# Performance work log

Measured on AMD Instinct MI355X. Metric: run time of the kernel, lower is better.

The kernel has to match this reference:

```python
import jax, jax.numpy as jnp
import numpy as np
from math import sqrt

D_MODEL = 768
N_HEADS = 12
D_K = 64
D_V = 64
LN_EPS = 1e-5
NEG = -1e9


def layer_norm(x, g, b):
    mu = jnp.mean(x, axis=-1, keepdims=True)
    var = jnp.mean((x - mu) ** 2, axis=-1, keepdims=True)
    return (x - mu) * jax.lax.rsqrt(var + LN_EPS) * g + b


def setup_inputs() -> dict:
    key = jax.random.key(0)
    ks = jax.random.split(key, 8)
    B, S = 4, 1024
    pro1 = jax.random.normal(ks[0], (B, S, D_MODEL), dtype=jnp.float32)
    pro2 = jax.random.normal(ks[1], (B, S, D_MODEL), dtype=jnp.float32)
    # attn_mask is [B, H, S2, S1]; transpose(2,3) masks scores [B,H,S1,S2]
    mask1_2 = jax.random.bernoulli(ks[2], 0.3, (B, N_HEADS, S, S))
    sc = 1.0 / np.sqrt(D_MODEL)
    W_Q = jax.random.normal(ks[3], (D_MODEL, D_K * N_HEADS), dtype=jnp.float32) * sc
    W_K = jax.random.normal(ks[4], (D_MODEL, D_K * N_HEADS), dtype=jnp.float32) * sc
    fc1 = jax.random.normal(ks[5], (D_V * N_HEADS, D_MODEL), dtype=jnp.float32) * sc
    g1 = jnp.ones((D_MODEL,), jnp.float32)
    b1 = jnp.zeros((D_MODEL,), jnp.float32)
    g2 = jnp.ones((D_MODEL,), jnp.float32)
    b2 = jnp.zeros((D_MODEL,), jnp.float32)
    return {"pro1": pro1, "pro2": pro2, "mask1_2": mask1_2,
            "W_Q": W_Q, "W_K": W_K, "fc1": fc1,
            "g1": g1, "b1": b1, "g2": g2, "b2": b2}


def reference(pro1, pro2, mask1_2, W_Q, W_K, fc1, g1, b1, g2, b2):
    B, S1, _ = pro1.shape
    S2 = pro2.shape[1]
    # project and split heads: [B, H, S, d_k]
    Q = (pro1 @ W_Q).reshape(B, S1, N_HEADS, D_K).transpose(0, 2, 1, 3)
    K = (pro2 @ W_K).reshape(B, S2, N_HEADS, D_K).transpose(0, 2, 1, 3)
    scores = jnp.einsum('bhsd,bhtd->bhst', Q, K) / sqrt(D_K)  # [B,H,S1,S2]
    mask = jnp.swapaxes(mask1_2, 2, 3)  # attn_mask.transpose(2,3)
    scores = jnp.where(mask, NEG, scores)
    attn1 = jax.nn.softmax(scores, axis=-1)                  # over S2
    attn2 = jax.nn.softmax(jnp.swapaxes(scores, -1, -2), axis=-1)  # over S1
    ctx1 = jnp.einsum('bhst,bhtd->bhsd', attn1, K)  # [B,H,S1,d_k]
    ctx2 = jnp.einsum('bhts,bhsd->bhtd', attn2, Q)  # [B,H,S2,d_k]
    c1 = ctx1.transpose(0, 2, 1, 3).reshape(B, S1, N_HEADS * D_V)
    c2 = ctx2.transpose(0, 2, 1, 3).reshape(B, S2, N_HEADS * D_V)
    # NOTE: original applies fc1 to BOTH branches (fc2 is dead code)
    o1 = layer_norm(c1 @ fc1, g1, b1)
    o2 = layer_norm(c2 @ fc1, g2, b2)
    return (o1, o2)
```

## Files before the change

### kernel.cpp

```cpp
#include <hip/hip_runtime.h>
#include <hip/hip_bf16.h>
#include <stdint.h>

#define S 1024
#define DMODEL 768
#define NH 12
#define DK 64
#define BB 4
#define BH 48
#define M4 4096

typedef __attribute__((ext_vector_type(8))) short bf16x8;
typedef __attribute__((ext_vector_type(4))) float f32x4;
typedef __attribute__((ext_vector_type(4))) _Float16 f16x4;
typedef __attribute__((ext_vector_type(8))) _Float16 f16x8;

static __device__ __forceinline__ unsigned short f2bf(float f) {
  unsigned int u = __float_as_uint(f);
  unsigned int r = u + 0x7FFFu + ((u >> 16) & 1u);
  return (unsigned short)(r >> 16);
}
static __device__ __forceinline__ unsigned int pk2(float a, float b) {
  return (unsigned int)f2bf(a) | ((unsigned int)f2bf(b) << 16);
}
static __device__ __forceinline__ bf16x8 ldfrag(const unsigned short* p) {
  uint4 q = *reinterpret_cast<const uint4*>(p);
  return __builtin_bit_cast(bf16x8, q);
}
static __device__ __forceinline__ f16x8 ldfragh(const unsigned short* p) {
  uint4 q = *reinterpret_cast<const uint4*>(p);
  return __builtin_bit_cast(f16x8, q);
}
static __device__ __forceinline__ unsigned short h2u(_Float16 h) {
  return __builtin_bit_cast(unsigned short, h);
}

__global__ __launch_bounds__(256) void k_transpose(const float* w0, const float* w1, const float* w2,
                                                   unsigned short* o0, unsigned short* o1, unsigned short* o2) {
  const float* in = blockIdx.z == 0 ? w0 : (blockIdx.z == 1 ? w1 : w2);
  unsigned short* out = blockIdx.z == 0 ? o0 : (blockIdx.z == 1 ? o1 : o2);
  __shared__ float tile[32][33];
  int n0 = blockIdx.x * 32, k0 = blockIdx.y * 32;
  int tid = threadIdx.x;
  int r = tid >> 3, c = (tid & 7) * 4;
  float4 v = *reinterpret_cast<const float4*>(in + (size_t)(k0 + r) * DMODEL + n0 + c);
  tile[r][c] = v.x; tile[r][c + 1] = v.y; tile[r][c + 2] = v.z; tile[r][c + 3] = v.w;
  __syncthreads();
  ushort4 o;
  o.x = f2bf(tile[c + 0][r]);
  o.y = f2bf(tile[c + 1][r]);
  o.z = f2bf(tile[c + 2][r]);
  o.w = f2bf(tile[c + 3][r]);
  *reinterpret_cast<ushort4*>(out + (size_t)(n0 + r) * DMODEL + k0 + c) = o;
}

__global__ __launch_bounds__(256) void k_pack(const int* __restrict__ mask,
                                              unsigned int* __restrict__ mp2) {
  int bh = blockIdx.y;
  int w = threadIdx.x >> 6, lane = threadIdx.x & 63;
  int tile = blockIdx.x * 4 + w;
  int ti = tile >> 4, tj = tile & 15;
  int t0 = ti * 64, s0 = tj * 64;
  const int* mb = mask + (size_t)bh * S * S;
  unsigned long long rowword = 0;
#pragma unroll 8
  for (int r = 0; r < 64; ++r) {
    int v = mb[(size_t)(t0 + r) * S + s0 + lane];
    unsigned long long b = __ballot(v != 0);
    if (lane == r) rowword = b;
  }
  unsigned int* p2 = mp2 + (size_t)bh * 32 * S;
  p2[((s0 >> 5) + 0) * S + t0 + lane] = (unsigned int)rowword;
  p2[((s0 >> 5) + 1) * S + t0 + lane] = (unsigned int)(rowword >> 32);
}

__global__ __launch_bounds__(256, 2) void k_gemm128(
    int mode,
    const float* __restrict__ Af0, const float* __restrict__ Af1,
    const unsigned short* __restrict__ Ab0, const unsigned short* __restrict__ Ab1,
    const unsigned short* __restrict__ Bt0, const unsigned short* __restrict__ Bt1,
    unsigned short* __restrict__ oQ0, unsigned short* __restrict__ oQ1,
    unsigned short* __restrict__ oT0, unsigned short* __restrict__ oT1,
    float* __restrict__ oF0, float* __restrict__ oF1) {
  const float* Af = blockIdx.z ? Af1 : Af0;
  const unsigned short* Ab = blockIdx.z ? Ab1 : Ab0;
  const unsigned short* Bt = blockIdx.z ? Bt1 : Bt0;
  __shared__ __align__(16) unsigned short As[128 * 72];
  __shared__ __align__(16) unsigned short Bs[128 * 72];
  int tid = threadIdx.x;
  int m0 = blockIdx.x * 128, n0 = blockIdx.y * 128;
  int w = tid >> 6, lane = tid & 63, lane15 = lane & 15, quad = lane >> 4;
  int row0 = (w >> 1) * 64, col0 = (w & 1) * 64;
  f32x4 acc[4][4] = {};
  int sr = tid >> 2, sc = (tid & 3) * 16;
  const unsigned short* gB0 = Bt + (size_t)(n0 + sr) * DMODEL + sc;
  const unsigned short* gB1 = Bt + (size_t)(n0 + 64 + sr) * DMODEL + sc;
  uint4 vb[2][2];
  vb[0][0] = *reinterpret_cast<const uint4*>(gB0);
  vb[0][1] = *reinterpret_cast<const uint4*>(gB0 + 8);
  vb[1][0] = *reinterpret_cast<const uint4*>(gB1);
  vb[1][1] = *reinterpret_cast<const uint4*>(gB1 + 8);
  const float* gAf0 = Af + (size_t)(m0 + sr) * DMODEL + sc;
  const float* gAf1 = Af + (size_t)(m0 + 64 + sr) * DMODEL + sc;
  const unsigned short* gAb0 = Ab + (size_t)(m0 + sr) * DMODEL + sc;
  const unsigned short* gAb1 = Ab + (size_t)(m0 + 64 + sr) * DMODEL + sc;
  float4 fa[2][4];
  uint4 va[2][2];
  if (mode == 0) {
#pragma unroll
    for (int g = 0; g < 4; ++g) fa[0][g] = *reinterpret_cast<const float4*>(gAf0 + g * 4);
#pragma unroll
    for (int g = 0; g < 4; ++g) fa[1][g] = *reinterpret_cast<const float4*>(gAf1 + g * 4);
  } else {
    va[0][0] = *reinterpret_cast<const uint4*>(gAb0);
    va[0][1] = *reinterpret_cast<const uint4*>(gAb0 + 8);
    va[1][0] = *reinterpret_cast<const uint4*>(gAb1);
    va[1][1] = *reinterpret_cast<const uint4*>(gAb1 + 8);
  }
  for (int kc = 0; kc < 12; ++kc) {
    __syncthreads();
    if (mode == 0) {
#pragma unroll
      for (int h2 = 0; h2 < 2; ++h2) {
        uint4 u0, u1;
        u0.x = pk2(fa[h2][0].x, fa[h2][0].y); u0.y = pk2(fa[h2][0].z, fa[h2][0].w);
        u0.z = pk2(fa[h2][1].x, fa[h2][1].y); u0.w = pk2(fa[h2][1].z, fa[h2][1].w);
        u1.x = pk2(fa[h2][2].x, fa[h2][2].y); u1.y = pk2(fa[h2][2].z, fa[h2][2].w);
        u1.z = pk2(fa[h2][3].x, fa[h2][3].y); u1.w = pk2(fa[h2][3].z, fa[h2][3].w);
        *reinterpret_cast<uint4*>(&As[(h2 * 64 + sr) * 72 + sc]) = u0;
        *reinterpret_cast<uint4*>(&As[(h2 * 64 + sr) * 72 + sc + 8]) = u1;
      }
    } else {
#pragma unroll
      for (int h2 = 0; h2 < 2; ++h2) {
        *reinterpret_cast<uint4*>(&As[(h2 * 64 + sr) * 72 + sc]) = va[h2][0];
        *reinterpret_cast<uint4*>(&As[(h2 * 64 + sr) * 72 + sc + 8]) = va[h2][1];
      }
    }
#pragma unroll
    for (int h2 = 0; h2 < 2; ++h2) {
      *reinterpret_cast<uint4*>(&Bs[(h2 * 64 + sr) * 72 + sc]) = vb[h2][0];
      *reinterpret_cast<uint4*>(&Bs[(h2 * 64 + sr) * 72 + sc + 8]) = vb[h2][1];
    }
    if (kc < 11) {
      int k0 = (kc + 1) * 64;
      if (mode == 0) {
#pragma unroll
        for (int g = 0; g < 4; ++g) fa[0][g] = *reinterpret_cast<const float4*>(gAf0 + k0 + g * 4);
#pragma unroll
        for (int g = 0; g < 4; ++g) fa[1][g] = *reinterpret_cast<const float4*>(gAf1 + k0 + g * 4);
      } else {
        va[0][0] = *reinterpret_cast<const uint4*>(gAb0 + k0);
        va[0][1] = *reinterpret_cast<const uint4*>(gAb0 + k0 + 8);
        va[1][0] = *reinterpret_cast<const uint4*>(gAb1 + k0);
        va[1][1] = *reinterpret_cast<const uint4*>(gAb1 + k0 + 8);
      }
      vb[0][0] = *reinterpret_cast<const uint4*>(gB0 + k0);
      vb[0][1] = *reinterpret_cast<const uint4*>(gB0 + k0 + 8);
      vb[1][0] = *reinterpret_cast<const uint4*>(gB1 + k0);
      vb[1][1] = *reinterpret_cast<const uint4*>(gB1 + k0 + 8);
    }
    __syncthreads();
#pragma unroll
    for (int ks = 0; ks < 2; ++ks) {
      int kk = ks * 32 + quad * 8;
      bf16x8 a[4], b[4];
#pragma unroll
      for (int i = 0; i < 4; ++i) a[i] = ldfrag(&As[(row0 + i * 16 + lane15) * 72 + kk]);
#pragma unroll
      for (int j = 0; j < 4; ++j) b[j] = ldfrag(&Bs[(col0 + j * 16 + lane15) * 72 + kk]);
#pragma unroll
      for (int i = 0; i < 4; ++i)
#pragma unroll
        for (int j = 0; j < 4; ++j)
          acc[i][j] = __builtin_amdgcn_mfma_f32_16x16x32_bf16(a[i], b[j], acc[i][j], 0, 0, 0);
    }
  }
  if (mode == 0) {
    unsigned short* out = blockIdx.z ? oQ1 : oQ0;
    unsigned short* outT = blockIdx.z ? oT1 : oT0;
    f16x4 iden;
#pragma unroll
    for (int i = 0; i < 4; ++i) iden[i] = (_Float16)((quad * 4 + i) == lane15 ? 1.0f : 0.0f);
    f32x4 zero4 = {};
#pragma unroll
    for (int i = 0; i < 4; ++i)
#pragma unroll
      for (int j = 0; j < 4; ++j) {
        f16x4 cf;
#pragma unroll
        for (int reg = 0; reg < 4; ++reg) cf[reg] = (_Float16)acc[i][j][reg];
        f32x4 tq = __builtin_amdgcn_mfma_f32_16x16x16f16(cf, iden, zero4, 0, 0, 0);
        {
          int m = m0 + row0 + i * 16 + lane15;
          int n = n0 + col0 + j * 16 + quad * 4;
          int b = m >> 10, s = m & 1023, h = n >> 6, d = n & 63;
          ushort4 o;
          o.x = h2u((_Float16)tq[0]); o.y = h2u((_Float16)tq[1]);
          o.z = h2u((_Float16)tq[2]); o.w = h2u((_Float16)tq[3]);
          *reinterpret_cast<ushort4*>(&out[(((size_t)(b * NH + h)) * S + s) * DK + d]) = o;
        }
        {
          int n = n0 + col0 + j * 16 + lane15;
          int m = m0 + row0 + i * 16 + quad * 4;
          int b = m >> 10, s = m & 1023, h = n >> 6, d = n & 63;
          ushort4 o;
          o.x = h2u((_Float16)acc[i][j][0]); o.y = h2u((_Float16)acc[i][j][1]);
          o.z = h2u((_Float16)acc[i][j][2]); o.w = h2u((_Float16)acc[i][j][3]);
          *reinterpret_cast<ushort4*>(&outT[(((size_t)(b * NH + h)) * DK + d) * S + s]) = o;
        }
      }
  } else {
    float* out = blockIdx.z ? oF1 : oF0;
#pragma unroll
    for (int i = 0; i < 4; ++i)
#pragma unroll
      for (int j = 0; j < 4; ++j)
#pragma unroll
        for (int reg = 0; reg < 4; ++reg) {
          int m = m0 + row0 + i * 16 + quad * 4 + reg;
          int n = n0 + col0 + j * 16 + lane15;
          out[(size_t)m * DMODEL + n] = acc[i][j][reg];
        }
  }
}

__global__ __launch_bounds__(256, 3) void k_attn(
    const unsigned short* __restrict__ Qb, const unsigned short* __restrict__ Kb,
    const unsigned short* __restrict__ QT, const unsigned short* __restrict__ KT,
    const unsigned int* __restrict__ mp2,
    unsigned short* __restrict__ c1, unsigned short* __restrict__ c2) {
  int bh = blockIdx.y, path = blockIdx.z;
  int s0b = blockIdx.x * 128;
  const unsigned short* X = path ? Kb : Qb;
  const unsigned short* Y = path ? Qb : Kb;
  const unsigned short* YT = path ? QT : KT;
  unsigned short* outc = path ? c2 : c1;

  __shared__ __align__(16) unsigned short YS[64 * 72];
  __shared__ __align__(16) unsigned short YTS[64 * 72];
  __shared__ unsigned int MWS[256];

  const unsigned short* Xb = X + (size_t)bh * S * DK;
  const unsigned short* Yb = Y + (size_t)bh * S * DK;
  const unsigned short* YTb = YT + (size_t)bh * DK * S;
  const unsigned int* mbg = mp2 + (size_t)bh * 32 * S;

  int tid = threadIdx.x;
  int w = tid >> 6, lane = tid & 63, lane15 = lane & 15, quad = lane >> 4;
  int s0w = s0b + w * 32;

  f16x8 xf[2][2];
#pragma unroll
  for (int rg = 0; rg < 2; ++rg) {
    xf[rg][0] = ldfragh(Xb + (size_t)(s0w + rg * 16 + lane15) * DK + quad * 8);
    xf[rg][1] = ldfragh(Xb + (size_t)(s0w + rg * 16 + lane15) * DK + 32 + quad * 8);
  }

  int sr4 = tid >> 2, sc4 = (tid & 3) * 16;
  const unsigned short* gY = Yb + (size_t)sr4 * DK + sc4;
  const unsigned short* gYT = YTb + (size_t)sr4 * S + sc4;
  uint4 y0 = *reinterpret_cast<const uint4*>(gY);
  uint4 y1 = *reinterpret_cast<const uint4*>(gY + 8);
  uint4 t0 = *reinterpret_cast<const uint4*>(gYT);
  uint4 t1 = *reinterpret_cast<const uint4*>(gYT + 8);
  int mws_idx = (path == 0) ? ((tid & 63) * 4 + (tid >> 6)) : ((tid & 127) * 2 + (tid >> 7));
  unsigned int mwv = (path == 0)
      ? mbg[((size_t)((s0b >> 5) + (tid >> 6))) * S + (tid & 63)]
      : mbg[((size_t)(tid >> 7)) * S + s0b + (tid & 127)];

  f32x4 outa[2][4] = {};
  float lsum[2] = {0.f, 0.f};

  for (int jc = 0; jc < 16; ++jc) {
    __syncthreads();
    *reinterpret_cast<uint4*>(&YS[sr4 * 72 + sc4]) = y0;
    *reinterpret_cast<uint4*>(&YS[sr4 * 72 + sc4 + 8]) = y1;
    *reinterpret_cast<uint4*>(&YTS[sr4 * 72 + sc4]) = t0;
    *reinterpret_cast<uint4*>(&YTS[sr4 * 72 + sc4 + 8]) = t1;
    MWS[mws_idx] = mwv;
    {
      int jn = (jc + 1 < 16) ? (jc + 1) * 64 : jc * 64;
      y0 = *reinterpret_cast<const uint4*>(gY + (size_t)jn * DK);
      y1 = *reinterpret_cast<const uint4*>(gY + (size_t)jn * DK + 8);
      t0 = *reinterpret_cast<const uint4*>(gYT + jn);
      t1 = *reinterpret_cast<const uint4*>(gYT + jn + 8);
      mwv = (path == 0)
          ? mbg[((size_t)((s0b >> 5) + (tid >> 6))) * S + jn + (tid & 63)]
          : mbg[((size_t)((jn >> 5) + (tid >> 7))) * S + s0b + (tid & 127)];
    }
    __syncthreads();

    f32x4 scv[4][2];
#pragma unroll
    for (int st = 0; st < 4; ++st) {
      f16x8 a0 = ldfragh(&YS[(st * 16 + lane15) * 72 + quad * 8]);
      f16x8 a1 = ldfragh(&YS[(st * 16 + lane15) * 72 + 32 + quad * 8]);
#pragma unroll
      for (int rg = 0; rg < 2; ++rg) {
        f32x4 v = {};
        v = __builtin_amdgcn_mfma_f32_16x16x32_f16(a0, xf[rg][0], v, 0, 0, 0);
        v = __builtin_amdgcn_mfma_f32_16x16x32_f16(a1, xf[rg][1], v, 0, 0, 0);
        scv[st][rg] = v;
      }
    }
    f16x4 pfa[4][2];
    if (path == 0) {
#pragma unroll
      for (int st = 0; st < 4; ++st)
#pragma unroll
        for (int reg = 0; reg < 4; ++reg) {
          unsigned int wdv = MWS[(st * 16 + quad * 4 + reg) * 4 + w];
#pragma unroll
          for (int rg = 0; rg < 2; ++rg) {
            float e = __expf(scv[st][rg][reg] * 0.125f);
            float p = ((wdv >> (unsigned)(rg * 16 + lane15)) & 1u) ? 0.f : e;
            lsum[rg] += p;
            pfa[st][rg][reg] = (_Float16)p;
          }
        }
    } else {
#pragma unroll
      for (int rg = 0; rg < 2; ++rg) {
        unsigned int wv0 = MWS[(w * 32 + rg * 16 + lane15) * 2 + 0];
        unsigned int wv1 = MWS[(w * 32 + rg * 16 + lane15) * 2 + 1];
#pragma unroll
        for (int st = 0; st < 4; ++st) {
          unsigned int wdv = (st < 2) ? wv0 : wv1;
#pragma unroll
          for (int reg = 0; reg < 4; ++reg) {
            unsigned int sh = (unsigned)((st & 1) * 16 + quad * 4 + reg);
            float e = __expf(scv[st][rg][reg] * 0.125f);
            float p = ((wdv >> sh) & 1u) ? 0.f : e;
            lsum[rg] += p;
            pfa[st][rg][reg] = (_Float16)p;
          }
        }
      }
    }
#pragma unroll
    for (int st = 0; st < 4; ++st)
#pragma unroll
      for (int dsub = 0; dsub < 4; ++dsub) {
        uint2 q = *reinterpret_cast<const uint2*>(&YTS[(dsub * 16 + lane15) * 72 + st * 16 + quad * 4]);
        f16x4 yb = __builtin_bit_cast(f16x4, q);
#pragma unroll
        for (int rg = 0; rg < 2; ++rg)
          outa[rg][dsub] = __builtin_amdgcn_mfma_f32_16x16x16f16(pfa[st][rg], yb, outa[rg][dsub], 0, 0, 0);
      }
  }

#pragma unroll
  for (int rg = 0; rg < 2; ++rg) {
    lsum[rg] += __shfl_xor(lsum[rg], 16);
    lsum[rg] += __shfl_xor(lsum[rg], 32);
  }
  float rinv[2][4];
#pragma unroll
  for (int rg = 0; rg < 2; ++rg)
#pragma unroll
    for (int reg = 0; reg < 4; ++reg)
      rinv[rg][reg] = 1.0f / __shfl(lsum[rg], quad * 4 + reg);

  int b = bh / NH, h = bh % NH;
#pragma unroll
  for (int rg = 0; rg < 2; ++rg)
#pragma unroll
    for (int dsub = 0; dsub < 4; ++dsub)
#pragma unroll
      for (int reg = 0; reg < 4; ++reg) {
        float v = outa[rg][dsub][reg] * rinv[rg][reg];
        int srow = s0w + rg * 16 + quad * 4 + reg;
        size_t idx = ((size_t)(b * S) + srow) * DMODEL + h * DK + dsub * 16 + lane15;
        outc[idx] = f2bf(v);
      }
}

__global__ __launch_bounds__(256) void k_ln(const float* __restrict__ f1, const float* __restrict__ f2,
                                            const float* __restrict__ g1, const float* __restrict__ b1,
                                            const float* __restrict__ g2, const float* __restrict__ b2,
                                            float* __restrict__ out) {
  int rowg = blockIdx.x;
  int sel = rowg >> 12;
  int row = rowg & 4095;
  const float* in = sel ? f2 : f1;
  const float* g = sel ? g2 : g1;
  const float* be = sel ? b2 : b1;
  int tid = threadIdx.x;
  const float* p = in + (size_t)row * DMODEL;
  float x0 = p[tid], x1 = p[tid + 256], x2 = p[tid + 512];
  float s = x0 + x1 + x2;
  float ss = x0 * x0 + x1 * x1 + x2 * x2;
#pragma unroll
  for (int m = 1; m < 64; m <<= 1) { s += __shfl_xor(s, m); ss += __shfl_xor(ss, m); }
  __shared__ float ps[4], pss[4];
  int w = tid >> 6;
  if ((tid & 63) == 0) { ps[w] = s; pss[w] = ss; }
  __syncthreads();
  s = ps[0] + ps[1] + ps[2] + ps[3];
  ss = pss[0] + pss[1] + pss[2] + pss[3];
  float mu = s * (1.0f / 768.0f);
  float var = ss * (1.0f / 768.0f) - mu * mu;
  float rstd = rsqrtf(var + 1e-5f);
  float* o = out + ((size_t)sel * M4 + row) * DMODEL;
  o[tid] = (x0 - mu) * rstd * g[tid] + be[tid];
  o[tid + 256] = (x1 - mu) * rstd * g[tid + 256] + be[tid + 256];
  o[tid + 512] = (x2 - mu) * rstd * g[tid + 512] + be[tid + 512];
}

extern "C" void kernel_launch(void* const* d_in, const int* in_sizes, int n_in,
                              void* d_out, int out_size, void* d_ws, size_t ws_size,
                              hipStream_t stream) {
  const float* pro1 = (const float*)d_in[0];
  const float* pro2 = (const float*)d_in[1];
  const int* mask = (const int*)d_in[2];
  const float* WQ = (const float*)d_in[3];
  const float* WK = (const float*)d_in[4];
  const float* FC1 = (const float*)d_in[5];
  const float* g1 = (const float*)d_in[6];
  const float* b1 = (const float*)d_in[7];
  const float* g2 = (const float*)d_in[8];
  const float* b2 = (const float*)d_in[9];
  float* out = (float*)d_out;
  char* ws = (char*)d_ws;

  float* f1 = (float*)(ws + 0);
  unsigned short* wqt = (unsigned short*)(ws + 12582912);
  unsigned short* wkt = (unsigned short*)(ws + 13762560);
  unsigned short* fc1t = (unsigned short*)(ws + 14942208);
  unsigned short* Qb = (unsigned short*)(ws + 16121856);
  unsigned short* Kb = (unsigned short*)(ws + 22413312);
  unsigned short* QT = (unsigned short*)(ws + 28704768);
  unsigned short* KT = (unsigned short*)(ws + 34996224);
  unsigned int* mp2 = (unsigned int*)(ws + 41287680);
  float* f2 = (float*)(ws + 47579136);
  unsigned short* c1 = (unsigned short*)(ws + 60162048);
  unsigned short* c2 = (unsigned short*)(ws + 66453504);

  k_transpose<<<dim3(24, 24, 3), 256, 0, stream>>>(WQ, WK, FC1, wqt, wkt, fc1t);
  k_pack<<<dim3(64, BH), 256, 0, stream>>>(mask, mp2);
  k_gemm128<<<dim3(32, 6, 2), 256, 0, stream>>>(0, pro1, pro2, nullptr, nullptr, wqt, wkt,
                                                Qb, Kb, QT, KT, nullptr, nullptr);
  k_attn<<<dim3(8, BH, 2), 256, 0, stream>>>(Qb, Kb, QT, KT, mp2, c1, c2);
  k_gemm128<<<dim3(32, 6, 2), 256, 0, stream>>>(1, nullptr, nullptr, c1, c2, fc1t, fc1t,
                                                nullptr, nullptr, nullptr, nullptr, f1, f2);
  k_ln<<<8192, 256, 0, stream>>>(f1, f2, g1, b1, g2, b2, out);
}
```

Baseline: 474.4 us.

## Shrink GEMM and attention tiles, pre-convert inputs to bf16

The fp32 activations are now converted to bf16 in a separate pass, so the projection GEMM loads bf16 directly. The GEMM M tile is halved to 64 rows and the attention query tile to 64 rows (16 per wave), with launch bounds raised to 4 blocks per CU. This doubles the number of blocks and cuts per-thread register use, aiming for more occupancy and better CU fill on the large chip. The cost is two extra conversion launches, an extra read/write of the inputs, and more re-reading of the B/K tiles across the larger grid.

```diff
diff --git a/kernel.cpp b/kernel.cpp
--- a/kernel.cpp
+++ b/kernel.cpp
@@ -20,9 +20,6 @@
   unsigned int r = u + 0x7FFFu + ((u >> 16) & 1u);
   return (unsigned short)(r >> 16);
 }
-static __device__ __forceinline__ unsigned int pk2(float a, float b) {
-  return (unsigned int)f2bf(a) | ((unsigned int)f2bf(b) << 16);
-}
 static __device__ __forceinline__ bf16x8 ldfrag(const unsigned short* p) {
   uint4 q = *reinterpret_cast<const uint4*>(p);
   return __builtin_bit_cast(bf16x8, q);
@@ -33,6 +30,17 @@
 }
 static __device__ __forceinline__ unsigned short h2u(_Float16 h) {
   return __builtin_bit_cast(unsigned short, h);
+}
+
+__global__ __launch_bounds__(256) void k_convert(const float* __restrict__ in,
+                                                 unsigned short* __restrict__ out, int n4) {
+  int i = blockIdx.x * 256 + threadIdx.x;
+  if (i < n4) {
+    float4 v = reinterpret_cast<const float4*>(in)[i];
+    ushort4 o;
+    o.x = f2bf(v.x); o.y = f2bf(v.y); o.z = f2bf(v.z); o.w = f2bf(v.w);
+    reinterpret_cast<ushort4*>(out)[i] = o;
+  }
 }
 
 __global__ __launch_bounds__(256) void k_transpose(const float* w0, const float* w1, const float* w2,
@@ -74,87 +82,45 @@
   p2[((s0 >> 5) + 1) * S + t0 + lane] = (unsigned int)(rowword >> 32);
 }
 
-__global__ __launch_bounds__(256, 2) void k_gemm128(
+__global__ __launch_bounds__(256, 4) void k_gemm(
     int mode,
-    const float* __restrict__ Af0, const float* __restrict__ Af1,
-    const unsigned short* __restrict__ Ab0, const unsigned short* __restrict__ Ab1,
+    const unsigned short* __restrict__ A0, const unsigned short* __restrict__ A1,
     const unsigned short* __restrict__ Bt0, const unsigned short* __restrict__ Bt1,
     unsigned short* __restrict__ oQ0, unsigned short* __restrict__ oQ1,
     unsigned short* __restrict__ oT0, unsigned short* __restrict__ oT1,
     float* __restrict__ oF0, float* __restrict__ oF1) {
-  const float* Af = blockIdx.z ? Af1 : Af0;
-  const unsigned short* Ab = blockIdx.z ? Ab1 : Ab0;
+  const unsigned short* A = blockIdx.z ? A1 : A0;
   const unsigned short* Bt = blockIdx.z ? Bt1 : Bt0;
-  __shared__ __align__(16) unsigned short As[128 * 72];
+  __shared__ __align__(16) unsigned short As[64 * 72];
   __shared__ __align__(16) unsigned short Bs[128 * 72];
   int tid = threadIdx.x;
-  int m0 = blockIdx.x * 128, n0 = blockIdx.y * 128;
+  int m0 = blockIdx.x * 64, n0 = blockIdx.y * 128;
   int w = tid >> 6, lane = tid & 63, lane15 = lane & 15, quad = lane >> 4;
-  int row0 = (w >> 1) * 64, col0 = (w & 1) * 64;
-  f32x4 acc[4][4] = {};
+  int row0 = (w >> 1) * 32, col0 = (w & 1) * 64;
+  f32x4 acc[2][4] = {};
   int sr = tid >> 2, sc = (tid & 3) * 16;
+  const unsigned short* gA = A + (size_t)(m0 + sr) * DMODEL + sc;
   const unsigned short* gB0 = Bt + (size_t)(n0 + sr) * DMODEL + sc;
   const unsigned short* gB1 = Bt + (size_t)(n0 + 64 + sr) * DMODEL + sc;
+  uint4 va0 = *reinterpret_cast<const uint4*>(gA);
+  uint4 va1 = *reinterpret_cast<const uint4*>(gA + 8);
   uint4 vb[2][2];
   vb[0][0] = *reinterpret_cast<const uint4*>(gB0);
   vb[0][1] = *reinterpret_cast<const uint4*>(gB0 + 8);
   vb[1][0] = *reinterpret_cast<const uint4*>(gB1);
   vb[1][1] = *reinterpret_cast<const uint4*>(gB1 + 8);
-  const float* gAf0 = Af + (size_t)(m0 + sr) * DMODEL + sc;
-  const float* gAf1 = Af + (size_t)(m0 + 64 + sr) * DMODEL + sc;
-  const unsigned short* gAb0 = Ab + (size_t)(m0 + sr) * DMODEL + sc;
-  const unsigned short* gAb1 = Ab + (size_t)(m0 + 64 + sr) * DMODEL + sc;
-  float4 fa[2][4];
-  uint4 va[2][2];
-  if (mode == 0) {
-#pragma unroll
-    for (int g = 0; g < 4; ++g) fa[0][g] = *reinterpret_cast<const float4*>(gAf0 + g * 4);
-#pragma unroll
-    for (int g = 0; g < 4; ++g) fa[1][g] = *reinterpret_cast<const float4*>(gAf1 + g * 4);
-  } else {
-    va[0][0] = *reinterpret_cast<const uint4*>(gAb0);
-    va[0][1] = *reinterpret_cast<const uint4*>(gAb0 + 8);
-    va[1][0] = *reinterpret_cast<const uint4*>(gAb1);
-    va[1][1] = *reinterpret_cast<const uint4*>(gAb1 + 8);
-  }
   for (int kc = 0; kc < 12; ++kc) {
     __syncthreads();
-    if (mode == 0) {
-#pragma unroll
-      for (int h2 = 0; h2 < 2; ++h2) {
-        uint4 u0, u1;
-        u0.x = pk2(fa[h2][0].x, fa[h2][0].y); u0.y = pk2(fa[h2][0].z, fa[h2][0].w);
-        u0.z = pk2(fa[h2][1].x, fa[h2][1].y); u0.w = pk2(fa[h2][1].z, fa[h2][1].w);
-        u1.x = pk2(fa[h2][2].x, fa[h2][2].y); u1.y = pk2(fa[h2][2].z, fa[h2][2].w);
-        u1.z = pk2(fa[h2][3].x, fa[h2][3].y); u1.w = pk2(fa[h2][3].z, fa[h2][3].w);
-        *reinterpret_cast<uint4*>(&As[(h2 * 64 + sr) * 72 + sc]) = u0;
-        *reinterpret_cast<uint4*>(&As[(h2 * 64 + sr) * 72 + sc + 8]) = u1;
-      }
-    } else {
-#pragma unroll
-      for (int h2 = 0; h2 < 2; ++h2) {
-        *reinterpret_cast<uint4*>(&As[(h2 * 64 + sr) * 72 + sc]) = va[h2][0];
-        *reinterpret_cast<uint4*>(&As[(h2 * 64 + sr) * 72 + sc + 8]) = va[h2][1];
-      }
-    }
-#pragma unroll
-    for (int h2 = 0; h2 < 2; ++h2) {
-      *reinterpret_cast<uint4*>(&Bs[(h2 * 64 + sr) * 72 + sc]) = vb[h2][0];
-      *reinterpret_cast<uint4*>(&Bs[(h2 * 64 + sr) * 72 + sc + 8]) = vb[h2][1];
-    }
+    *reinterpret_cast<uint4*>(&As[sr * 72 + sc]) = va0;
+    *reinterpret_cast<uint4*>(&As[sr * 72 + sc + 8]) = va1;
+    *reinterpret_cast<uint4*>(&Bs[sr * 72 + sc]) = vb[0][0];
+    *reinterpret_cast<uint4*>(&Bs[sr * 72 + sc + 8]) = vb[0][1];
+    *reinterpret_cast<uint4*>(&Bs[(64 + sr) * 72 + sc]) = vb[1][0];
+    *reinterpret_cast<uint4*>(&Bs[(64 + sr) * 72 + sc + 8]) = vb[1][1];
     if (kc < 11) {
       int k0 = (kc + 1) * 64;
-      if (mode == 0) {
-#pragma unroll
-        for (int g = 0; g < 4; ++g) fa[0][g] = *reinterpret_cast<const float4*>(gAf0 + k0 + g * 4);
-#pragma unroll
-        for (int g = 0; g < 4; ++g) fa[1][g] = *reinterpret_cast<const float4*>(gAf1 + k0 + g * 4);
-      } else {
-        va[0][0] = *reinterpret_cast<const uint4*>(gAb0 + k0);
-        va[0][1] = *reinterpret_cast<const uint4*>(gAb0 + k0 + 8);
-        va[1][0] = *reinterpret_cast<const uint4*>(gAb1 + k0);
-        va[1][1] = *reinterpret_cast<const uint4*>(gAb1 + k0 + 8);
-      }
+      va0 = *reinterpret_cast<const uint4*>(gA + k0);
+      va1 = *reinterpret_cast<const uint4*>(gA + k0 + 8);
       vb[0][0] = *reinterpret_cast<const uint4*>(gB0 + k0);
       vb[0][1] = *reinterpret_cast<const uint4*>(gB0 + k0 + 8);
       vb[1][0] = *reinterpret_cast<const uint4*>(gB1 + k0);
@@ -164,13 +130,13 @@
 #pragma unroll
     for (int ks = 0; ks < 2; ++ks) {
       int kk = ks * 32 + quad * 8;
-      bf16x8 a[4], b[4];
-#pragma unroll
-      for (int i = 0; i < 4; ++i) a[i] = ldfrag(&As[(row0 + i * 16 + lane15) * 72 + kk]);
+      bf16x8 a[2], b[4];
+#pragma unroll
+      for (int i = 0; i < 2; ++i) a[i] = ldfrag(&As[(row0 + i * 16 + lane15) * 72 + kk]);
 #pragma unroll
       for (int j = 0; j < 4; ++j) b[j] = ldfrag(&Bs[(col0 + j * 16 + lane15) * 72 + kk]);
 #pragma unroll
-      for (int i = 0; i < 4; ++i)
+      for (int i = 0; i < 2; ++i)
 #pragma unroll
         for (int j = 0; j < 4; ++j)
           acc[i][j] = __builtin_amdgcn_mfma_f32_16x16x32_bf16(a[i], b[j], acc[i][j], 0, 0, 0);
@@ -184,7 +150,7 @@
     for (int i = 0; i < 4; ++i) iden[i] = (_Float16)((quad * 4 + i) == lane15 ? 1.0f : 0.0f);
     f32x4 zero4 = {};
 #pragma unroll
-    for (int i = 0; i < 4; ++i)
+    for (int i = 0; i < 2; ++i)
 #pragma unroll
       for (int j = 0; j < 4; ++j) {
         f16x4 cf;
@@ -213,7 +179,7 @@
   } else {
     float* out = blockIdx.z ? oF1 : oF0;
 #pragma unroll
-    for (int i = 0; i < 4; ++i)
+    for (int i = 0; i < 2; ++i)
 #pragma unroll
       for (int j = 0; j < 4; ++j)
 #pragma unroll
@@ -225,13 +191,13 @@
   }
 }
 
-__global__ __launch_bounds__(256, 3) void k_attn(
+__global__ __launch_bounds__(256, 4) void k_attn(
     const unsigned short* __restrict__ Qb, const unsigned short* __restrict__ Kb,
     const unsigned short* __restrict__ QT, const unsigned short* __restrict__ KT,
     const unsigned int* __restrict__ mp2,
     unsigned short* __restrict__ c1, unsigned short* __restrict__ c2) {
   int bh = blockIdx.y, path = blockIdx.z;
-  int s0b = blockIdx.x * 128;
+  int s0b = blockIdx.x * 64;
   const unsigned short* X = path ? Kb : Qb;
   const unsigned short* Y = path ? Qb : Kb;
   const unsigned short* YT = path ? QT : KT;
@@ -239,7 +205,7 @@
 
   __shared__ __align__(16) unsigned short YS[64 * 72];
   __shared__ __align__(16) unsigned short YTS[64 * 72];
-  __shared__ unsigned int MWS[256];
+  __shared__ unsigned int MWS[128];
 
   const unsigned short* Xb = X + (size_t)bh * S * DK;
   const unsigned short* Yb = Y + (size_t)bh * S * DK;
@@ -248,14 +214,10 @@
 
   int tid = threadIdx.x;
   int w = tid >> 6, lane = tid & 63, lane15 = lane & 15, quad = lane >> 4;
-  int s0w = s0b + w * 32;
-
-  f16x8 xf[2][2];
-#pragma unroll
-  for (int rg = 0; rg < 2; ++rg) {
-    xf[rg][0] = ldfragh(Xb + (size_t)(s0w + rg * 16 + lane15) * DK + quad * 8);
-    xf[rg][1] = ldfragh(Xb + (size_t)(s0w + rg * 16 + lane15) * DK + 32 + quad * 8);
-  }
+  int s0w = s0b + w * 16;
+
+  f16x8 xf0 = ldfragh(Xb + (size_t)(s0w + lane15) * DK + quad * 8);
+  f16x8 xf1 = ldfragh(Xb + (size_t)(s0w + lane15) * DK + 32 + quad * 8);
 
   int sr4 = tid >> 2, sc4 = (tid & 3) * 16;
   const unsigned short* gY = Yb + (size_t)sr4 * DK + sc4;
@@ -264,13 +226,14 @@
   uint4 y1 = *reinterpret_cast<const uint4*>(gY + 8);
   uint4 t0 = *reinterpret_cast<const uint4*>(gYT);
   uint4 t1 = *reinterpret_cast<const uint4*>(gYT + 8);
-  int mws_idx = (path == 0) ? ((tid & 63) * 4 + (tid >> 6)) : ((tid & 127) * 2 + (tid >> 7));
-  unsigned int mwv = (path == 0)
-      ? mbg[((size_t)((s0b >> 5) + (tid >> 6))) * S + (tid & 63)]
-      : mbg[((size_t)(tid >> 7)) * S + s0b + (tid & 127)];
-
-  f32x4 outa[2][4] = {};
-  float lsum[2] = {0.f, 0.f};
+  unsigned int mwv = 0;
+  if (tid < 128)
+    mwv = (path == 0)
+        ? mbg[((size_t)((s0b >> 5) + (tid & 1))) * S + (tid >> 1)]
+        : mbg[((size_t)(tid & 1)) * S + s0b + (tid >> 1)];
+
+  f32x4 outa[4] = {};
+  float lsum = 0.f;
 
   for (int jc = 0; jc < 16; ++jc) {
     __syncthreads();
@@ -278,63 +241,56 @@
     *reinterpret_cast<uint4*>(&YS[sr4 * 72 + sc4 + 8]) = y1;
     *reinterpret_cast<uint4*>(&YTS[sr4 * 72 + sc4]) = t0;
     *reinterpret_cast<uint4*>(&YTS[sr4 * 72 + sc4 + 8]) = t1;
-    MWS[mws_idx] = mwv;
+    if (tid < 128) MWS[tid] = mwv;
     {
       int jn = (jc + 1 < 16) ? (jc + 1) * 64 : jc * 64;
       y0 = *reinterpret_cast<const uint4*>(gY + (size_t)jn * DK);
       y1 = *reinterpret_cast<const uint4*>(gY + (size_t)jn * DK + 8);
       t0 = *reinterpret_cast<const uint4*>(gYT + jn);
       t1 = *reinterpret_cast<const uint4*>(gYT + jn + 8);
-      mwv = (path == 0)
-          ? mbg[((size_t)((s0b >> 5) + (tid >> 6))) * S + jn + (tid & 63)]
-          : mbg[((size_t)((jn >> 5) + (tid >> 7))) * S + s0b + (tid & 127)];
+      if (tid < 128)
+        mwv = (path == 0)
+            ? mbg[((size_t)((s0b >> 5) + (tid & 1))) * S + jn + (tid >> 1)]
+            : mbg[((size_t)((jn >> 5) + (tid & 1))) * S + s0b + (tid >> 1)];
     }
     __syncthreads();
 
-    f32x4 scv[4][2];
+    f32x4 scv[4];
 #pragma unroll
     for (int st = 0; st < 4; ++st) {
       f16x8 a0 = ldfragh(&YS[(st * 16 + lane15) * 72 + quad * 8]);
       f16x8 a1 = ldfragh(&YS[(st * 16 + lane15) * 72 + 32 + quad * 8]);
-#pragma unroll
-      for (int rg = 0; rg < 2; ++rg) {
-        f32x4 v = {};
-        v = __builtin_amdgcn_mfma_f32_16x16x32_f16(a0, xf[rg][0], v, 0, 0, 0);
-        v = __builtin_amdgcn_mfma_f32_16x16x32_f16(a1, xf[rg][1], v, 0, 0, 0);
-        scv[st][rg] = v;
-      }
-    }
-    f16x4 pfa[4][2];
+      f32x4 v = {};
+      v = __builtin_amdgcn_mfma_f32_16x16x32_f16(a0, xf0, v, 0, 0, 0);
+      v = __builtin_amdgcn_mfma_f32_16x16x32_f16(a1, xf1, v, 0, 0, 0);
+      scv[st] = v;
+    }
+    f16x4 pfa[4];
     if (path == 0) {
+      unsigned int sh = (unsigned)((w & 1) * 16 + lane15);
 #pragma unroll
       for (int st = 0; st < 4; ++st)
 #pragma unroll
         for (int reg = 0; reg < 4; ++reg) {
-          unsigned int wdv = MWS[(st * 16 + quad * 4 + reg) * 4 + w];
-#pragma unroll
-          for (int rg = 0; rg < 2; ++rg) {
-            float e = __expf(scv[st][rg][reg] * 0.125f);
-            float p = ((wdv >> (unsigned)(rg * 16 + lane15)) & 1u) ? 0.f : e;
-            lsum[rg] += p;
-            pfa[st][rg][reg] = (_Float16)p;
-          }
+          unsigned int wdv = MWS[(st * 16 + quad * 4 + reg) * 2 + (w >> 1)];
+          float e = __expf(scv[st][reg] * 0.125f);
+          float p = ((wdv >> sh) & 1u) ? 0.f : e;
+          lsum += p;
+          pfa[st][reg] = (_Float16)p;
         }
     } else {
-#pragma unroll
-      for (int rg = 0; rg < 2; ++rg) {
-        unsigned int wv0 = MWS[(w * 32 + rg * 16 + lane15) * 2 + 0];
-        unsigned int wv1 = MWS[(w * 32 + rg * 16 + lane15) * 2 + 1];
-#pragma unroll
-        for (int st = 0; st < 4; ++st) {
-          unsigned int wdv = (st < 2) ? wv0 : wv1;
-#pragma unroll
-          for (int reg = 0; reg < 4; ++reg) {
-            unsigned int sh = (unsigned)((st & 1) * 16 + quad * 4 + reg);
-            float e = __expf(scv[st][rg][reg] * 0.125f);
-            float p = ((wdv >> sh) & 1u) ? 0.f : e;
-            lsum[rg] += p;
-            pfa[st][rg][reg] = (_Float16)p;
-          }
+      unsigned int wv0 = MWS[(w * 16 + lane15) * 2 + 0];
+      unsigned int wv1 = MWS[(w * 16 + lane15) * 2 + 1];
+#pragma unroll
+      for (int st = 0; st < 4; ++st) {
+        unsigned int wdv = (st < 2) ? wv0 : wv1;
+#pragma unroll
+        for (int reg = 0; reg < 4; ++reg) {
+          unsigned int sh = (unsigned)((st & 1) * 16 + quad * 4 + reg);
+          float e = __expf(scv[st][reg] * 0.125f);
+          float p = ((wdv >> sh) & 1u) ? 0.f : e;
+          lsum += p;
+          pfa[st][reg] = (_Float16)p;
         }
       }
     }
@@ -344,36 +300,27 @@
       for (int dsub = 0; dsub < 4; ++dsub) {
         uint2 q = *reinterpret_cast<const uint2*>(&YTS[(dsub * 16 + lane15) * 72 + st * 16 + quad * 4]);
         f16x4 yb = __builtin_bit_cast(f16x4, q);
-#pragma unroll
-        for (int rg = 0; rg < 2; ++rg)
-          outa[rg][dsub] = __builtin_amdgcn_mfma_f32_16x16x16f16(pfa[st][rg], yb, outa[rg][dsub], 0, 0, 0);
+        outa[dsub] = __builtin_amdgcn_mfma_f32_16x16x16f16(pfa[st], yb, outa[dsub], 0, 0, 0);
       }
   }
 
-#pragma unroll
-  for (int rg = 0; rg < 2; ++rg) {
-    lsum[rg] += __shfl_xor(lsum[rg], 16);
-    lsum[rg] += __shfl_xor(lsum[rg], 32);
-  }
-  float rinv[2][4];
-#pragma unroll
-  for (int rg = 0; rg < 2; ++rg)
-#pragma unroll
-    for (int reg = 0; reg < 4; ++reg)
-      rinv[rg][reg] = 1.0f / __shfl(lsum[rg], quad * 4 + reg);
+  lsum += __shfl_xor(lsum, 16);
+  lsum += __shfl_xor(lsum, 32);
+  float rinv[4];
+#pragma unroll
+  for (int reg = 0; reg < 4; ++reg)
+    rinv[reg] = 1.0f / __shfl(lsum, quad * 4 + reg);
 
   int b = bh / NH, h = bh % NH;
 #pragma unroll
-  for (int rg = 0; rg < 2; ++rg)
-#pragma unroll
-    for (int dsub = 0; dsub < 4; ++dsub)
-#pragma unroll
-      for (int reg = 0; reg < 4; ++reg) {
-        float v = outa[rg][dsub][reg] * rinv[rg][reg];
-        int srow = s0w + rg * 16 + quad * 4 + reg;
-        size_t idx = ((size_t)(b * S) + srow) * DMODEL + h * DK + dsub * 16 + lane15;
-        outc[idx] = f2bf(v);
-      }
+  for (int dsub = 0; dsub < 4; ++dsub)
+#pragma unroll
+    for (int reg = 0; reg < 4; ++reg) {
+      float v = outa[dsub][reg] * rinv[reg];
+      int srow = s0w + quad * 4 + reg;
+      size_t idx = ((size_t)(b * S) + srow) * DMODEL + h * DK + dsub * 16 + lane15;
+      outc[idx] = f2bf(v);
+    }
 }
 
 __global__ __launch_bounds__(256) void k_ln(const float* __restrict__ f1, const float* __restrict__ f2,
@@ -424,6 +371,8 @@
   float* out = (float*)d_out;
   char* ws = (char*)d_ws;
 
+  unsigned short* pro1b = (unsigned short*)(ws + 0);
+  unsigned short* pro2b = (unsigned short*)(ws + 6291456);
   float* f1 = (float*)(ws + 0);
   unsigned short* wqt = (unsigned short*)(ws + 12582912);
   unsigned short* wkt = (unsigned short*)(ws + 13762560);
@@ -437,12 +386,14 @@
   unsigned short* c1 = (unsigned short*)(ws + 60162048);
   unsigned short* c2 = (unsigned short*)(ws + 66453504);
 
+  k_convert<<<3072, 256, 0, stream>>>(pro1, pro1b, 786432);
+  k_convert<<<3072, 256, 0, stream>>>(pro2, pro2b, 786432);
   k_transpose<<<dim3(24, 24, 3), 256, 0, stream>>>(WQ, WK, FC1, wqt, wkt, fc1t);
   k_pack<<<dim3(64, BH), 256, 0, stream>>>(mask, mp2);
-  k_gemm128<<<dim3(32, 6, 2), 256, 0, stream>>>(0, pro1, pro2, nullptr, nullptr, wqt, wkt,
-                                                Qb, Kb, QT, KT, nullptr, nullptr);
-  k_attn<<<dim3(8, BH, 2), 256, 0, stream>>>(Qb, Kb, QT, KT, mp2, c1, c2);
-  k_gemm128<<<dim3(32, 6, 2), 256, 0, stream>>>(1, nullptr, nullptr, c1, c2, fc1t, fc1t,
-                                                nullptr, nullptr, nullptr, nullptr, f1, f2);
+  k_gemm<<<dim3(64, 6, 2), 256, 0, stream>>>(0, pro1b, pro2b, wqt, wkt,
+                                             Qb, Kb, QT, KT, nullptr, nullptr);
+  k_attn<<<dim3(16, BH, 2), 256, 0, stream>>>(Qb, Kb, QT, KT, mp2, c1, c2);
+  k_gemm<<<dim3(64, 6, 2), 256, 0, stream>>>(1, c1, c2, fc1t, fc1t,
+                                             nullptr, nullptr, nullptr, nullptr, f1, f2);
   k_ln<<<8192, 256, 0, stream>>>(f1, f2, g1, b1, g2, b2, out);
 }
```

Measured after the change: 496.1 us. 4.6% more time.

## Load GEMM tiles via direct global-to-LDS with XOR swizzle, pre-convert inputs to bf16

Applied to the files above, without the earlier changes.

The GEMM kernel now stages A and B tiles with global_load_lds straight into shared memory, using an XOR-swizzled unpadded layout instead of padded register-staged stores. Two new kernels convert pro1/pro2 to bf16 ahead of time so both GEMM modes read bf16 A. Occupancy is raised to 3 blocks per SM. The intent is to drop register staging and conversion work from the GEMM main loop. The cost is extra launches plus a full read and write of the inputs, and the loop loses register prefetch double-buffering: the next tile is loaded only after the compute on the current one finishes.

```diff
diff --git a/kernel.cpp b/kernel.cpp
--- a/kernel.cpp
+++ b/kernel.cpp
@@ -20,9 +20,6 @@
   unsigned int r = u + 0x7FFFu + ((u >> 16) & 1u);
   return (unsigned short)(r >> 16);
 }
-static __device__ __forceinline__ unsigned int pk2(float a, float b) {
-  return (unsigned int)f2bf(a) | ((unsigned int)f2bf(b) << 16);
-}
 static __device__ __forceinline__ bf16x8 ldfrag(const unsigned short* p) {
   uint4 q = *reinterpret_cast<const uint4*>(p);
   return __builtin_bit_cast(bf16x8, q);
@@ -33,6 +30,22 @@
 }
 static __device__ __forceinline__ unsigned short h2u(_Float16 h) {
   return __builtin_bit_cast(unsigned short, h);
+}
+static __device__ __forceinline__ void gl2lds16(const unsigned short* g, unsigned short* l) {
+  __builtin_amdgcn_global_load_lds(
+      (const __attribute__((address_space(1))) unsigned int*)g,
+      (__attribute__((address_space(3))) unsigned int*)l, 16, 0, 0);
+}
+
+__global__ __launch_bounds__(256) void k_convert(const float* __restrict__ in,
+                                                 unsigned short* __restrict__ out, int n4) {
+  int i = blockIdx.x * 256 + threadIdx.x;
+  if (i < n4) {
+    float4 v = reinterpret_cast<const float4*>(in)[i];
+    ushort4 o;
+    o.x = f2bf(v.x); o.y = f2bf(v.y); o.z = f2bf(v.z); o.w = f2bf(v.w);
+    reinterpret_cast<ushort4*>(out)[i] = o;
+  }
 }
 
 __global__ __launch_bounds__(256) void k_transpose(const float* w0, const float* w1, const float* w2,
@@ -74,108 +87,68 @@
   p2[((s0 >> 5) + 1) * S + t0 + lane] = (unsigned int)(rowword >> 32);
 }
 
-__global__ __launch_bounds__(256, 2) void k_gemm128(
+__global__ __launch_bounds__(256, 3) void k_gemm(
     int mode,
-    const float* __restrict__ Af0, const float* __restrict__ Af1,
-    const unsigned short* __restrict__ Ab0, const unsigned short* __restrict__ Ab1,
+    const unsigned short* __restrict__ A0, const unsigned short* __restrict__ A1,
     const unsigned short* __restrict__ Bt0, const unsigned short* __restrict__ Bt1,
     unsigned short* __restrict__ oQ0, unsigned short* __restrict__ oQ1,
     unsigned short* __restrict__ oT0, unsigned short* __restrict__ oT1,
     float* __restrict__ oF0, float* __restrict__ oF1) {
-  const float* Af = blockIdx.z ? Af1 : Af0;
-  const unsigned short* Ab = blockIdx.z ? Ab1 : Ab0;
+  const unsigned short* A = blockIdx.z ? A1 : A0;
   const unsigned short* Bt = blockIdx.z ? Bt1 : Bt0;
-  __shared__ __align__(16) unsigned short As[128 * 72];
-  __shared__ __align__(16) unsigned short Bs[128 * 72];
+  __shared__ __align__(16) unsigned short As[128 * 64];
+  __shared__ __align__(16) unsigned short Bs[128 * 64];
   int tid = threadIdx.x;
   int m0 = blockIdx.x * 128, n0 = blockIdx.y * 128;
   int w = tid >> 6, lane = tid & 63, lane15 = lane & 15, quad = lane >> 4;
   int row0 = (w >> 1) * 64, col0 = (w & 1) * 64;
   f32x4 acc[4][4] = {};
-  int sr = tid >> 2, sc = (tid & 3) * 16;
-  const unsigned short* gB0 = Bt + (size_t)(n0 + sr) * DMODEL + sc;
-  const unsigned short* gB1 = Bt + (size_t)(n0 + 64 + sr) * DMODEL + sc;
-  uint4 vb[2][2];
-  vb[0][0] = *reinterpret_cast<const uint4*>(gB0);
-  vb[0][1] = *reinterpret_cast<const uint4*>(gB0 + 8);
-  vb[1][0] = *reinterpret_cast<const uint4*>(gB1);
-  vb[1][1] = *reinterpret_cast<const uint4*>(gB1 + 8);
-  const float* gAf0 = Af + (size_t)(m0 + sr) * DMODEL + sc;
-  const float* gAf1 = Af + (size_t)(m0 + 64 + sr) * DMODEL + sc;
-  const unsigned short* gAb0 = Ab + (size_t)(m0 + sr) * DMODEL + sc;
-  const unsigned short* gAb1 = Ab + (size_t)(m0 + 64 + sr) * DMODEL + sc;
-  float4 fa[2][4];
-  uint4 va[2][2];
-  if (mode == 0) {
-#pragma unroll
-    for (int g = 0; g < 4; ++g) fa[0][g] = *reinterpret_cast<const float4*>(gAf0 + g * 4);
-#pragma unroll
-    for (int g = 0; g < 4; ++g) fa[1][g] = *reinterpret_cast<const float4*>(gAf1 + g * 4);
-  } else {
-    va[0][0] = *reinterpret_cast<const uint4*>(gAb0);
-    va[0][1] = *reinterpret_cast<const uint4*>(gAb0 + 8);
-    va[1][0] = *reinterpret_cast<const uint4*>(gAb1);
-    va[1][1] = *reinterpret_cast<const uint4*>(gAb1 + 8);
-  }
+
+  const unsigned short* gA[4];
+  const unsigned short* gB[4];
+  unsigned short* lA[4];
+  unsigned short* lB[4];
+  {
+    int lr = lane >> 3;
+    int ch = lane & 7;
+#pragma unroll
+    for (int i = 0; i < 4; ++i) {
+      int r = w * 32 + i * 8 + lr;
+      int cs = ((ch ^ (r & 7)) * 8);
+      gA[i] = A + (size_t)(m0 + r) * DMODEL + cs;
+      gB[i] = Bt + (size_t)(n0 + r) * DMODEL + cs;
+      lA[i] = &As[(w * 32 + i * 8) * 64];
+      lB[i] = &Bs[(w * 32 + i * 8) * 64];
+    }
+  }
+  int l7 = lane15 & 7;
+#pragma unroll
+  for (int i = 0; i < 4; ++i) { gl2lds16(gA[i], lA[i]); gl2lds16(gB[i], lB[i]); }
+
   for (int kc = 0; kc < 12; ++kc) {
     __syncthreads();
-    if (mode == 0) {
-#pragma unroll
-      for (int h2 = 0; h2 < 2; ++h2) {
-        uint4 u0, u1;
-        u0.x = pk2(fa[h2][0].x, fa[h2][0].y); u0.y = pk2(fa[h2][0].z, fa[h2][0].w);
-        u0.z = pk2(fa[h2][1].x, fa[h2][1].y); u0.w = pk2(fa[h2][1].z, fa[h2][1].w);
-        u1.x = pk2(fa[h2][2].x, fa[h2][2].y); u1.y = pk2(fa[h2][2].z, fa[h2][2].w);
-        u1.z = pk2(fa[h2][3].x, fa[h2][3].y); u1.w = pk2(fa[h2][3].z, fa[h2][3].w);
-        *reinterpret_cast<uint4*>(&As[(h2 * 64 + sr) * 72 + sc]) = u0;
-        *reinterpret_cast<uint4*>(&As[(h2 * 64 + sr) * 72 + sc + 8]) = u1;
-      }
-    } else {
-#pragma unroll
-      for (int h2 = 0; h2 < 2; ++h2) {
-        *reinterpret_cast<uint4*>(&As[(h2 * 64 + sr) * 72 + sc]) = va[h2][0];
-        *reinterpret_cast<uint4*>(&As[(h2 * 64 + sr) * 72 + sc + 8]) = va[h2][1];
-      }
-    }
-#pragma unroll
-    for (int h2 = 0; h2 < 2; ++h2) {
-      *reinterpret_cast<uint4*>(&Bs[(h2 * 64 + sr) * 72 + sc]) = vb[h2][0];
-      *reinterpret_cast<uint4*>(&Bs[(h2 * 64 + sr) * 72 + sc + 8]) = vb[h2][1];
-    }
-    if (kc < 11) {
-      int k0 = (kc + 1) * 64;
-      if (mode == 0) {
-#pragma unroll
-        for (int g = 0; g < 4; ++g) fa[0][g] = *reinterpret_cast<const float4*>(gAf0 + k0 + g * 4);
-#pragma unroll
-        for (int g = 0; g < 4; ++g) fa[1][g] = *reinterpret_cast<const float4*>(gAf1 + k0 + g * 4);
-      } else {
-        va[0][0] = *reinterpret_cast<const uint4*>(gAb0 + k0);
-        va[0][1] = *reinterpret_cast<const uint4*>(gAb0 + k0 + 8);
-        va[1][0] = *reinterpret_cast<const uint4*>(gAb1 + k0);
-        va[1][1] = *reinterpret_cast<const uint4*>(gAb1 + k0 + 8);
-      }
-      vb[0][0] = *reinterpret_cast<const uint4*>(gB0 + k0);
-      vb[0][1] = *reinterpret_cast<const uint4*>(gB0 + k0 + 8);
-      vb[1][0] = *reinterpret_cast<const uint4*>(gB1 + k0);
-      vb[1][1] = *reinterpret_cast<const uint4*>(gB1 + k0 + 8);
-    }
-    __syncthreads();
 #pragma unroll
     for (int ks = 0; ks < 2; ++ks) {
-      int kk = ks * 32 + quad * 8;
+      int co = (((ks * 4 + quad) ^ l7) * 8);
       bf16x8 a[4], b[4];
 #pragma unroll
-      for (int i = 0; i < 4; ++i) a[i] = ldfrag(&As[(row0 + i * 16 + lane15) * 72 + kk]);
-#pragma unroll
-      for (int j = 0; j < 4; ++j) b[j] = ldfrag(&Bs[(col0 + j * 16 + lane15) * 72 + kk]);
+      for (int i = 0; i < 4; ++i) a[i] = ldfrag(&As[(row0 + i * 16 + lane15) * 64 + co]);
+#pragma unroll
+      for (int j = 0; j < 4; ++j) b[j] = ldfrag(&Bs[(col0 + j * 16 + lane15) * 64 + co]);
 #pragma unroll
       for (int i = 0; i < 4; ++i)
 #pragma unroll
         for (int j = 0; j < 4; ++j)
           acc[i][j] = __builtin_amdgcn_mfma_f32_16x16x32_bf16(a[i], b[j], acc[i][j], 0, 0, 0);
     }
-  }
+    __syncthreads();
+    if (kc < 11) {
+      int ko = (kc + 1) * 64;
+#pragma unroll
+      for (int i = 0; i < 4; ++i) { gl2lds16(gA[i] + ko, lA[i]); gl2lds16(gB[i] + ko, lB[i]); }
+    }
+  }
+
   if (mode == 0) {
     unsigned short* out = blockIdx.z ? oQ1 : oQ0;
     unsigned short* outT = blockIdx.z ? oT1 : oT0;
@@ -424,6 +397,8 @@
   float* out = (float*)d_out;
   char* ws = (char*)d_ws;
 
+  unsigned short* pro1b = (unsigned short*)(ws + 0);
+  unsigned short* pro2b = (unsigned short*)(ws + 6291456);
   float* f1 = (float*)(ws + 0);
   unsigned short* wqt = (unsigned short*)(ws + 12582912);
   unsigned short* wkt = (unsigned short*)(ws + 13762560);
@@ -437,12 +412,14 @@
   unsigned short* c1 = (unsigned short*)(ws + 60162048);
   unsigned short* c2 = (unsigned short*)(ws + 66453504);
 
+  k_convert<<<3072, 256, 0, stream>>>(pro1, pro1b, 786432);
+  k_convert<<<3072, 256, 0, stream>>>(pro2, pro2b, 786432);
   k_transpose<<<dim3(24, 24, 3), 256, 0, stream>>>(WQ, WK, FC1, wqt, wkt, fc1t);
   k_pack<<<dim3(64, BH), 256, 0, stream>>>(mask, mp2);
-  k_gemm128<<<dim3(32, 6, 2), 256, 0, stream>>>(0, pro1, pro2, nullptr, nullptr, wqt, wkt,
-                                                Qb, Kb, QT, KT, nullptr, nullptr);
+  k_gemm<<<dim3(32, 6, 2), 256, 0, stream>>>(0, pro1b, pro2b, wqt, wkt,
+                                             Qb, Kb, QT, KT, nullptr, nullptr);
   k_attn<<<dim3(8, BH, 2), 256, 0, stream>>>(Qb, Kb, QT, KT, mp2, c1, c2);
-  k_gemm128<<<dim3(32, 6, 2), 256, 0, stream>>>(1, nullptr, nullptr, c1, c2, fc1t, fc1t,
-                                                nullptr, nullptr, nullptr, nullptr, f1, f2);
+  k_gemm<<<dim3(32, 6, 2), 256, 0, stream>>>(1, c1, c2, fc1t, fc1t,
+                                             nullptr, nullptr, nullptr, nullptr, f1, f2);
   k_ln<<<8192, 256, 0, stream>>>(f1, f2, g1, b1, g2, b2, out);
 }
```

Measured after the change: 415.6 us. 12.4% less time.
